# Kernel tuning notes

Measured on AMD Instinct MI355X. Metric: run time of the kernel, lower is better.

## Reference

```python
import jax, jax.numpy as jnp
import numpy as np

FEAT = 512      # feat_dim
HID = 256       # feat_dim // 2
K = 4           # DSL knn k
NCLS = 2
BUF = 8192      # rehearsal buffer size
B_BAGS = 8
N_INST = 16384


def _lin_init(k, i, o):
    return jax.random.normal(k, (i, o), jnp.float32) / np.sqrt(i)


def setup_inputs() -> dict:
    key = jax.random.key(0)
    ks = jax.random.split(key, 16)
    p = {}
    p['x'] = jax.random.normal(ks[0], (B_BAGS, N_INST, FEAT), jnp.float32)
    p['rehearsal'] = jax.random.uniform(ks[1], (BUF, FEAT), jnp.float32)
    # attention MIL pooling MLP
    p['aW1'] = _lin_init(ks[2], FEAT, FEAT); p['ab1'] = jnp.zeros((FEAT,), jnp.float32)
    p['aW2'] = _lin_init(ks[3], FEAT, 1);    p['ab2'] = jnp.zeros((1,), jnp.float32)
    # bag classifier
    p['cW'] = _lin_init(ks[4], FEAT, NCLS);  p['cb'] = jnp.zeros((NCLS,), jnp.float32)
    # DSL fc
    p['dW1'] = _lin_init(ks[5], FEAT, HID);  p['db1'] = jnp.zeros((HID,), jnp.float32)
    p['dW2'] = _lin_init(ks[6], HID, FEAT);  p['db2'] = jnp.zeros((FEAT,), jnp.float32)
    # GCN: hgc1 / hgc2 (HypergraphConv, heads=1, use_attention)
    p['g1W'] = _lin_init(ks[7], FEAT, FEAT)
    p['g1att'] = jax.random.normal(ks[8], (2 * FEAT,), jnp.float32) * 0.05
    p['g1b'] = jnp.zeros((FEAT,), jnp.float32)
    p['n1w'] = jnp.ones((FEAT,), jnp.float32); p['n1b'] = jnp.zeros((FEAT,), jnp.float32); p['n1s'] = jnp.ones((FEAT,), jnp.float32)
    p['f1W'] = _lin_init(ks[9], FEAT, HID);  p['f1b'] = jnp.zeros((HID,), jnp.float32)
    p['g2W'] = _lin_init(ks[10], FEAT, FEAT)
    p['g2att'] = jax.random.normal(ks[11], (2 * FEAT,), jnp.float32) * 0.05
    p['g2b'] = jnp.zeros((FEAT,), jnp.float32)
    p['n2w'] = jnp.ones((FEAT,), jnp.float32); p['n2b'] = jnp.zeros((FEAT,), jnp.float32); p['n2s'] = jnp.ones((FEAT,), jnp.float32)
    p['f2W'] = _lin_init(ks[12], FEAT, HID); p['f2b'] = jnp.zeros((HID,), jnp.float32)
    p['clW'] = _lin_init(ks[13], HID, NCLS); p['clb'] = jnp.zeros((NCLS,), jnp.float32)
    return p


def _hconv(x, eattr, src, edst, W, att, bias, n):
    """PyG HypergraphConv, heads=1, use_attention=True, concat, dropout=0.
    src = hyperedge_index[0] (node ids), edst = hyperedge_index[1] (hyperedge ids)."""
    xs = x @ W            # [n, F] node features after lin
    ea = eattr @ W        # [n, F] hyperedge attrs after lin
    F = xs.shape[1]
    alpha = xs[src] @ att[:F] + ea[edst] @ att[F:]        # [E]
    alpha = jax.nn.leaky_relu(alpha, 0.2)
    # softmax grouped by node index (hyperedge_index[0])
    m = jax.ops.segment_max(alpha, src, num_segments=n)
    e = jnp.exp(alpha - m[src])
    s = jax.ops.segment_sum(e, src, num_segments=n)
    alpha = e / s[src]
    ones = jnp.ones_like(alpha)
    deg = jax.ops.segment_sum(ones, src, num_segments=n)   # node degree D
    Dinv = jnp.where(deg > 0, 1.0 / deg, 0.0)
    esz = jax.ops.segment_sum(ones, edst, num_segments=n)  # hyperedge size B
    Binv = jnp.where(esz > 0, 1.0 / esz, 0.0)
    # node -> hyperedge, then hyperedge -> node
    out_e = jax.ops.segment_sum((Binv[edst] * alpha)[:, None] * xs[src], edst, num_segments=n)
    out_n = jax.ops.segment_sum((Dinv[src] * alpha)[:, None] * out_e[edst], src, num_segments=n)
    return out_n + bias


def _gnorm(x, w, b, s, eps=1e-5):
    # PyG GraphNorm, single graph
    mu = jnp.mean(x, axis=0)
    o = x - mu * s
    var = jnp.mean(o * o, axis=0)
    return w * o / jnp.sqrt(var + eps) + b


def reference(x, rehearsal, aW1, ab1, aW2, ab2, cW, cb, dW1, db1, dW2, db2,
              g1W, g1att, g1b, n1w, n1b, n1s, f1W, f1b,
              g2W, g2att, g2b, n2w, n2b, n2s, f2W, f2b, clW, clb):
    B = x.shape[0]
    # attention MIL pooling
    h = jax.nn.relu(x @ aW1 + ab1)                 # [B, N, F]
    scores = (h @ aW2 + ab2)[..., 0]               # [B, N]
    A = jax.nn.softmax(scores, axis=-1)
    M = jnp.einsum('bn,bnd->bd', A, x)             # [B, F]
    logits_mlp = M @ cW + cb
    # concat with rehearsal buffer -> graph nodes
    xc = jnp.concatenate([M, rehearsal], axis=0)   # [B+BUF, F]
    # DSL fc
    xg = jax.nn.leaky_relu(xc @ dW1 + db1, 0.01)
    xg = jax.nn.leaky_relu(xg @ dW2 + db2, 0.01)
    n = xg.shape[0]
    # cosine KNN (includes self, as torch_cluster.knn(x, x))
    xn = xg / (jnp.linalg.norm(xg, axis=1, keepdims=True) + 1e-12)
    sim = xn @ xn.T                                 # [n, n]
    _, nbr = jax.lax.top_k(sim, K)                  # [n, K]
    src = nbr.reshape(-1)                           # neighbor node ids
    edst = jnp.repeat(jnp.arange(n), K)             # hyperedge ids (query nodes)
    # scatter_mean of neighbor features per hyperedge (each has exactly K members)
    eattr = jnp.mean(xg[nbr], axis=1)               # [n, F]
    # GCN with hypergraph convs
    x1 = _hconv(xg, eattr, src, edst, g1W, g1att, g1b, n)
    x1 = jax.nn.leaky_relu(_gnorm(x1, n1w, n1b, n1s), 0.01)
    out = jax.nn.leaky_relu(x1 @ f1W + f1b, 0.01)
    x2 = _hconv(x1, eattr, src, edst, g2W, g2att, g2b, n)
    x2 = jax.nn.leaky_relu(_gnorm(x2, n2w, n2b, n2s), 0.01)
    out = out + jax.nn.leaky_relu(x2 @ f2W + f2b, 0.01)
    logits = out @ clW + clb
    logits_graph = logits[:B]
    return logits_mlp, logits_graph
```

## Files before the change

kernel.cpp:

```cpp
#include <hip/hip_runtime.h>
#include <math.h>
#include <limits.h>

#define FDIM 512
#define HIDN 256
#define NBAGS 8
#define NINST 16384
#define NNODE 8200
#define NEDGE 32800
#define BFSPLIT 8
#define MCHUNK 128

typedef __attribute__((ext_vector_type(8))) short short8v;
typedef __attribute__((ext_vector_type(4))) float f32x4v;

__device__ __forceinline__ float lrelu(float v, float s){ return v >= 0.f ? v : v*s; }

__device__ __forceinline__ void ins4(float v, int id, float* tv, int* ti){
    if ((v > tv[3]) || (v == tv[3] && id < ti[3])){
        tv[3]=v; ti[3]=id;
#pragma unroll
        for (int q=3;q>0;--q){
            bool sw = (tv[q] > tv[q-1]) || (tv[q]==tv[q-1] && ti[q]<ti[q-1]);
            if (sw){ float f=tv[q]; tv[q]=tv[q-1]; tv[q-1]=f; int d=ti[q]; ti[q]=ti[q-1]; ti[q-1]=d; }
        }
    }
}

__device__ __forceinline__ void ins8(float v, int id, float* tv, int* ti){
    if ((v > tv[7]) || (v == tv[7] && id < ti[7])){
        tv[7]=v; ti[7]=id;
#pragma unroll
        for (int q=7;q>0;--q){
            bool sw = (tv[q] > tv[q-1]) || (tv[q]==tv[q-1] && ti[q]<ti[q-1]);
            if (sw){ float f=tv[q]; tv[q]=tv[q-1]; tv[q-1]=f; int d=ti[q]; ti[q]=ti[q-1]; ti[q-1]=d; }
        }
    }
}

__device__ __forceinline__ unsigned short f2bf(float f){
    unsigned u = __float_as_uint(f);
    unsigned r = u + 0x7FFFu + ((u >> 16) & 1u);
    return (unsigned short)(r >> 16);
}
__device__ __forceinline__ float bf2f(unsigned short h){
    return __uint_as_float((unsigned)h << 16);
}

__global__ void k_wsplit(const float* __restrict__ W,
        unsigned short* __restrict__ WThi, unsigned short* __restrict__ WTlo){
    int i = blockIdx.x*256 + threadIdx.x;
    int k = i >> 9, n = i & 511;
    float w = W[i];
    unsigned short hi = f2bf(w);
    unsigned short lo = f2bf(w - bf2f(hi));
    WThi[(size_t)n*512 + k] = hi;
    WTlo[(size_t)n*512 + k] = lo;
}

__global__ __launch_bounds__(256) void k_scores(const float* __restrict__ X,
        const unsigned short* __restrict__ WThi, const unsigned short* __restrict__ WTlo,
        const float* __restrict__ b1, const float* __restrict__ v2,
        float* __restrict__ scoresP)
{
    __shared__ unsigned short Ahi[128][40];
    __shared__ unsigned short Alo[128][40];
    __shared__ unsigned short Bhi[128][40];
    __shared__ unsigned short Blo[128][40];
    int t = threadIdx.x;
    int wv = t >> 6, lane = t & 63;
    int lcol = lane & 15, lk = lane >> 4;
    size_t mb = (size_t)blockIdx.y * 128;
    int nb = blockIdx.x * 128;

    f32x4v acc[2][8];
#pragma unroll
    for (int rf=0;rf<2;rf++)
#pragma unroll
        for (int cf=0;cf<8;cf++) acc[rf][cf] = (f32x4v){0.f,0.f,0.f,0.f};

    for (int kc = 0; kc < 512; kc += 32){
        __syncthreads();
#pragma unroll
        for (int q=0;q<4;q++){
            int idx = q*256 + t;
            int seg = idx & 7, row = idx >> 3;
            float4 v = *(const float4*)(X + (mb+row)*512 + kc + seg*4);
            ushort4 h, l;
            h.x=f2bf(v.x); h.y=f2bf(v.y); h.z=f2bf(v.z); h.w=f2bf(v.w);
            l.x=f2bf(v.x-bf2f(h.x)); l.y=f2bf(v.y-bf2f(h.y));
            l.z=f2bf(v.z-bf2f(h.z)); l.w=f2bf(v.w-bf2f(h.w));
            *(ushort4*)&Ahi[row][seg*4] = h;
            *(ushort4*)&Alo[row][seg*4] = l;
        }
#pragma unroll
        for (int q=0;q<2;q++){
            int idx = q*256 + t;
            int col = idx >> 2, part = idx & 3;
            *(short8v*)&Bhi[col][part*8] =
                *(const short8v*)(WThi + (size_t)(nb+col)*512 + kc + part*8);
            *(short8v*)&Blo[col][part*8] =
                *(const short8v*)(WTlo + (size_t)(nb+col)*512 + kc + part*8);
        }
        __syncthreads();
        int r0 = wv*32;
        short8v ah0 = *(const short8v*)&Ahi[r0      + lcol][lk*8];
        short8v al0 = *(const short8v*)&Alo[r0      + lcol][lk*8];
        short8v ah1 = *(const short8v*)&Ahi[r0 + 16 + lcol][lk*8];
        short8v al1 = *(const short8v*)&Alo[r0 + 16 + lcol][lk*8];
#pragma unroll
        for (int cf=0; cf<8; cf++){
            short8v bh = *(const short8v*)&Bhi[cf*16 + lcol][lk*8];
            short8v bl = *(const short8v*)&Blo[cf*16 + lcol][lk*8];
            acc[0][cf] = __builtin_amdgcn_mfma_f32_16x16x32_bf16(ah0, bh, acc[0][cf], 0,0,0);
            acc[0][cf] = __builtin_amdgcn_mfma_f32_16x16x32_bf16(ah0, bl, acc[0][cf], 0,0,0);
            acc[0][cf] = __builtin_amdgcn_mfma_f32_16x16x32_bf16(al0, bh, acc[0][cf], 0,0,0);
            acc[1][cf] = __builtin_amdgcn_mfma_f32_16x16x32_bf16(ah1, bh, acc[1][cf], 0,0,0);
            acc[1][cf] = __builtin_amdgcn_mfma_f32_16x16x32_bf16(ah1, bl, acc[1][cf], 0,0,0);
            acc[1][cf] = __builtin_amdgcn_mfma_f32_16x16x32_bf16(al1, bh, acc[1][cf], 0,0,0);
        }
    }
    float rowsum[2][4];
#pragma unroll
    for (int rf=0;rf<2;rf++)
#pragma unroll
        for (int r=0;r<4;r++) rowsum[rf][r]=0.f;
#pragma unroll
    for (int rf=0; rf<2; rf++)
#pragma unroll
        for (int cf=0; cf<8; cf++){
            int gc = nb + cf*16 + lcol;
            float bb = b1[gc], vv = v2[gc];
#pragma unroll
            for (int r=0;r<4;r++){
                float h = acc[rf][cf][r] + bb;
                h = h > 0.f ? h : 0.f;
                rowsum[rf][r] = fmaf(h, vv, rowsum[rf][r]);
            }
        }
#pragma unroll
    for (int mask=1; mask<16; mask<<=1)
#pragma unroll
        for (int rf=0;rf<2;rf++)
#pragma unroll
            for (int r=0;r<4;r++)
                rowsum[rf][r] += __shfl_xor(rowsum[rf][r], mask);
    if (lcol == 0){
#pragma unroll
        for (int rf=0;rf<2;rf++)
#pragma unroll
            for (int r=0;r<4;r++){
                size_t grow = mb + wv*32 + rf*16 + lk*4 + r;
                scoresP[(size_t)blockIdx.x*(NBAGS*NINST) + grow] = rowsum[rf][r];
            }
    }
}

__global__ void k_scred(const float* __restrict__ sp, float* __restrict__ s){
    int r = blockIdx.x*256+threadIdx.x;
    if (r < NBAGS*NINST)
        s[r] = sp[r] + sp[NBAGS*NINST + r] + sp[2*NBAGS*NINST + r] + sp[3*NBAGS*NINST + r];
}

__global__ __launch_bounds__(256) void k_softmax(float* __restrict__ s0){
    int b = blockIdx.x; float* s = s0 + (size_t)b*NINST;
    __shared__ float red[256];
    int t = threadIdx.x;
    float m = -INFINITY;
    for (int i=t;i<NINST;i+=256) m = fmaxf(m, s[i]);
    red[t]=m; __syncthreads();
    for (int st=128; st>0; st>>=1){ if(t<st) red[t]=fmaxf(red[t],red[t+st]); __syncthreads(); }
    m = red[0]; __syncthreads();
    float sum=0.f;
    for (int i=t;i<NINST;i+=256) sum += __expf(s[i]-m);
    red[t]=sum; __syncthreads();
    for (int st=128; st>0; st>>=1){ if(t<st) red[t]+=red[t+st]; __syncthreads(); }
    float inv = 1.f/red[0];
    for (int i=t;i<NINST;i+=256) s[i] = __expf(s[i]-m)*inv;
}

__global__ __launch_bounds__(256) void k_M(const float* __restrict__ x,
        const float* __restrict__ A, float* __restrict__ MP){
    int b = blockIdx.y; int chunk = blockIdx.x;
    int n0 = chunk*(NINST/MCHUNK);
    __shared__ float As[NINST/MCHUNK];
    int t=threadIdx.x;
    if (t < NINST/MCHUNK) As[t] = A[(size_t)b*NINST+n0+t];
    __syncthreads();
    float a0=0.f, a1=0.f;
    const float* xb = x + ((size_t)b*NINST + n0)*FDIM;
    for (int n=0;n<NINST/MCHUNK;n++){
        float w = As[n];
        a0 = fmaf(w, xb[(size_t)n*FDIM + t],       a0);
        a1 = fmaf(w, xb[(size_t)n*FDIM + t + 256], a1);
    }
    MP[((size_t)chunk*NBAGS + b)*FDIM + t]       = a0;
    MP[((size_t)chunk*NBAGS + b)*FDIM + t + 256] = a1;
}

__global__ void k_Mred(const float* __restrict__ mp, float* __restrict__ M_){
    int b = blockIdx.x; int d = threadIdx.x;
    float s=0.f;
    for (int c=0;c<MCHUNK;c++) s += mp[((size_t)c*NBAGS+b)*FDIM + d];
    M_[b*FDIM+d]=s;
}

__global__ void k_logits_mlp(const float* __restrict__ M_, const float* __restrict__ cW,
        const float* __restrict__ cb, float* __restrict__ outp){
    int t = threadIdx.x;
    if (t < 16){
        int r=t>>1, c=t&1;
        float s=cb[c];
        for (int k=0;k<FDIM;k++) s = fmaf(M_[r*FDIM+k], cW[k*2+c], s);
        outp[r*2+c] = s;
    }
}

__global__ void k_xc(const float* __restrict__ M_, const float* __restrict__ reh, float* __restrict__ xc){
    size_t i = (size_t)blockIdx.x*256 + threadIdx.x;
    if (i >= (size_t)NNODE*FDIM) return;
    xc[i] = (i < (size_t)NBAGS*FDIM) ? M_[i] : reh[i - (size_t)NBAGS*FDIM];
}

__global__ __launch_bounds__(256) void k_gemm(const float* __restrict__ X,
        const float* __restrict__ W, const float* __restrict__ bias,
        float* __restrict__ C, unsigned short* __restrict__ Cbf,
        int M, int N, int K, float slope)
{
    __shared__ float As[32][68];
    __shared__ float Ws[32][128];
    int t = threadIdx.x; int tx = t & 15, ty = t >> 4;
    int mb = blockIdx.y * 64, nb = blockIdx.x * 128;
    float acc[4][8];
#pragma unroll
    for (int i=0;i<4;i++)
#pragma unroll
        for (int j=0;j<8;j++) acc[i][j]=0.f;

    int kq=(t&7)*4, m0=t>>3;
    int n4=(t&31)*4, k0=t>>5;
    for (int kc=0;kc<K;kc+=32){
#pragma unroll
        for (int mm=0;mm<2;mm++){
            int m = m0 + mm*32;
            int gr = mb + m; if (gr >= M) gr = M-1;
            float4 v = *(const float4*)(X + (size_t)gr*K + kc + kq);
            As[kq+0][m]=v.x; As[kq+1][m]=v.y; As[kq+2][m]=v.z; As[kq+3][m]=v.w;
        }
#pragma unroll
        for (int kk=0;kk<4;kk++){
            float4 v = *(const float4*)(W + (size_t)(kc+k0+kk*8)*N + nb + n4);
            *(float4*)&Ws[k0+kk*8][n4] = v;
        }
        __syncthreads();
#pragma unroll 4
        for (int k=0;k<32;k++){
            float4 a = *(const float4*)&As[k][ty*4];
            float4 b0 = *(const float4*)&Ws[k][tx*4];
            float4 b1 = *(const float4*)&Ws[k][64+tx*4];
            float av[4]={a.x,a.y,a.z,a.w};
            float bv[8]={b0.x,b0.y,b0.z,b0.w,b1.x,b1.y,b1.z,b1.w};
#pragma unroll
            for (int i=0;i<4;i++)
#pragma unroll
                for (int j=0;j<8;j++)
                    acc[i][j] = fmaf(av[i], bv[j], acc[i][j]);
        }
        __syncthreads();
    }
#pragma unroll
    for (int i=0;i<4;i++){
        int gr = mb + ty*4 + i;
        if (gr >= M) continue;
        float o[8];
#pragma unroll
        for (int j=0;j<8;j++){
            int gc = (j<4) ? (nb + tx*4 + j) : (nb + 64 + tx*4 + (j-4));
            float v = acc[i][j] + (bias ? bias[gc] : 0.f);
            o[j] = lrelu(v, slope);
        }
        float4 o0 = make_float4(o[0],o[1],o[2],o[3]);
        float4 o1 = make_float4(o[4],o[5],o[6],o[7]);
        *(float4*)(C + (size_t)gr*N + nb + tx*4)      = o0;
        *(float4*)(C + (size_t)gr*N + nb + 64 + tx*4) = o1;
        if (Cbf){
            ushort4 h0, h1;
            h0.x=f2bf(o[0]); h0.y=f2bf(o[1]); h0.z=f2bf(o[2]); h0.w=f2bf(o[3]);
            h1.x=f2bf(o[4]); h1.y=f2bf(o[5]); h1.z=f2bf(o[6]); h1.w=f2bf(o[7]);
            *(ushort4*)(Cbf + (size_t)gr*N + nb + tx*4)      = h0;
            *(ushort4*)(Cbf + (size_t)gr*N + nb + 64 + tx*4) = h1;
        }
    }
}

__global__ void k_rowdot(const float* __restrict__ X, const float* __restrict__ v,
        float* __restrict__ out, int K, int mode){
    int r = blockIdx.x; int t = threadIdx.x;
    const float* xr = X + (size_t)r*K;
    float s = 0.f;
    if (mode==1){ for (int k=t;k<K;k+=64){ float x_=xr[k]; s=fmaf(x_,x_,s);} }
    else        { for (int k=t;k<K;k+=64) s=fmaf(xr[k],v[k],s); }
    for (int off=32;off;off>>=1) s += __shfl_down(s, off);
    if (t==0) out[r] = (mode==1)? 1.f/(sqrtf(s)+1e-12f) : s;
}

__global__ void k_watt(const float* __restrict__ W, const float* __restrict__ att2, float* __restrict__ w2){
    int k = blockIdx.x; int t=threadIdx.x;
    float s=0.f;
    for (int j=t;j<FDIM;j+=64) s=fmaf(W[(size_t)k*FDIM+j], att2[j], s);
    for (int off=32;off;off>>=1) s += __shfl_down(s, off);
    if (t==0) w2[k]=s;
}

__global__ __launch_bounds__(256) void k_simbf(const unsigned short* __restrict__ xgh,
        const float* __restrict__ rn, float* __restrict__ candV, int* __restrict__ candI)
{
    __shared__ unsigned short Bs[16][520];
    int t = threadIdx.x;
    int wv = t >> 6, lane = t & 63;
    int lcol = lane & 15, lk = lane >> 4;
    int split = blockIdx.x;
    int r0 = blockIdx.y * 64 + wv * 16;

    short8v aF[16];
    {
        int arow = r0 + lcol; if (arow >= NNODE) arow = NNODE - 1;
        const unsigned short* ap = xgh + (size_t)arow * FDIM + lk * 8;
#pragma unroll
        for (int s = 0; s < 16; s++)
            aF[s] = *(const short8v*)(ap + s * 32);
    }

    int c0 = split * 1025;
    int cend = c0 + 1025;

    float tv[4][4]; int ti[4][4];
#pragma unroll
    for (int i=0;i<4;i++)
#pragma unroll
        for (int q=0;q<4;q++){ tv[i][q]=-INFINITY; ti[i][q]=INT_MAX; }

    int rho = t >> 4, seg = t & 15;

    for (int cc = c0; cc < cend; cc += 16){
        __syncthreads();
        {
            int gc = cc + rho; if (gc >= cend) gc = cend - 1;
            const unsigned short* bp = xgh + (size_t)gc * FDIM;
#pragma unroll
            for (int p = 0; p < 4; p++)
                *(short8v*)&Bs[rho][seg*8 + p*128] = *(const short8v*)(bp + seg*8 + p*128);
        }
        __syncthreads();

        f32x4v acc = {0.f, 0.f, 0.f, 0.f};
#pragma unroll
        for (int s = 0; s < 16; s++){
            short8v bF = *(const short8v*)&Bs[lcol][lk*8 + s*32];
            acc = __builtin_amdgcn_mfma_f32_16x16x32_bf16(aF[s], bF, acc, 0, 0, 0);
        }
        int gcol = cc + lcol;
        bool valid = gcol < cend;
        float rnc = valid ? rn[gcol] : 0.f;
#pragma unroll
        for (int i = 0; i < 4; i++){
            float v = valid ? acc[i] * rnc : -INFINITY;
            ins4(v, gcol, tv[i], ti[i]);
        }
    }

    float mv[4][8]; int mi[4][8];
#pragma unroll
    for (int i=0;i<4;i++){
#pragma unroll
        for (int q=0;q<4;q++){ mv[i][q]=tv[i][q]; mi[i][q]=ti[i][q]; }
#pragma unroll
        for (int q=4;q<8;q++){ mv[i][q]=-INFINITY; mi[i][q]=INT_MAX; }
    }
#pragma unroll
    for (int mask=1; mask<16; mask<<=1){
        float ov[4][8]; int oi[4][8];
#pragma unroll
        for (int i=0;i<4;i++)
#pragma unroll
            for (int q=0;q<8;q++){
                ov[i][q] = __shfl_xor(mv[i][q], mask);
                oi[i][q] = __shfl_xor(mi[i][q], mask);
            }
#pragma unroll
        for (int i=0;i<4;i++)
#pragma unroll
            for (int q=0;q<8;q++)
                ins8(ov[i][q], oi[i][q], mv[i], mi[i]);
    }
    if (lcol == 0){
#pragma unroll
        for (int i=0;i<4;i++){
            int grow = r0 + lk*4 + i;
            if (grow < NNODE){
#pragma unroll
                for (int q=0;q<8;q++){
                    candV[((size_t)grow*BFSPLIT + split)*8 + q] = mv[i][q];
                    candI[((size_t)grow*BFSPLIT + split)*8 + q] = mi[i][q];
                }
            }
        }
    }
}

__global__ __launch_bounds__(256) void k_rescore(const float* __restrict__ xg,
        const float* __restrict__ rn, const float* __restrict__ candV,
        const int* __restrict__ candI, int* __restrict__ nbr)
{
    __shared__ float Xr[4][512];
    __shared__ float Cs[256][17];
    __shared__ int   CrowS[256];
    int t = threadIdx.x;
    int wv = t >> 6, lane = t & 63;
    int r0 = blockIdx.x * 4;
    int r  = r0 + wv;
    int cid = candI[(size_t)r*64 + lane];
    float pv = candV[(size_t)r*64 + lane];
    bool ok = (pv != -INFINITY) && (cid >= 0) && (cid < NNODE);
    int crow = ok ? cid : 0;
    CrowS[t] = crow;
    {
        int rr = t >> 6; int c = t & 63;
        const float* xp = xg + (size_t)(r0+rr)*FDIM;
        *(float4*)&Xr[rr][c*4]       = *(const float4*)(xp + c*4);
        *(float4*)&Xr[rr][256 + c*4] = *(const float4*)(xp + 256 + c*4);
    }
    float dot = 0.f;
    for (int kc = 0; kc < 512; kc += 16){
        __syncthreads();
#pragma unroll
        for (int p = 0; p < 4; p++){
            int slot = p*64 + (t >> 2);
            int f = t & 3;
            float4 v = *(const float4*)(xg + (size_t)CrowS[slot]*FDIM + kc + f*4);
            float* dst = &Cs[slot][f*4];
            dst[0]=v.x; dst[1]=v.y; dst[2]=v.z; dst[3]=v.w;
        }
        __syncthreads();
#pragma unroll
        for (int k2 = 0; k2 < 16; k2++)
            dot = fmaf(Xr[wv][kc + k2], Cs[t][k2], dot);
    }
    float v = ok ? (dot * rn[r]) * rn[crow] : -INFINITY;
    int id = ok ? cid : INT_MAX;
    float tvv[4]={-INFINITY,-INFINITY,-INFINITY,-INFINITY};
    int tii[4]={INT_MAX,INT_MAX,INT_MAX,INT_MAX};
    ins4(v, id, tvv, tii);
#pragma unroll
    for (int mask=1; mask<64; mask<<=1){
        float ov[4]; int oi[4];
#pragma unroll
        for (int s=0;s<4;s++){ ov[s]=__shfl_xor(tvv[s],mask); oi[s]=__shfl_xor(tii[s],mask); }
#pragma unroll
        for (int s=0;s<4;s++) ins4(ov[s], oi[s], tvv, tii);
    }
    if (lane == 0){
#pragma unroll
        for (int s=0;s<4;s++) nbr[r*4+s] = tii[s];
    }
}

__global__ void k_eattr(const float* __restrict__ xg, const int* __restrict__ nbr, float* __restrict__ ea){
    int j = blockIdx.x; int t = threadIdx.x;
    int n0=nbr[j*4], n1=nbr[j*4+1], n2=nbr[j*4+2], n3=nbr[j*4+3];
    for (int d=t; d<FDIM; d+=256){
        float s = xg[(size_t)n0*FDIM+d]+xg[(size_t)n1*FDIM+d]+xg[(size_t)n2*FDIM+d]+xg[(size_t)n3*FDIM+d];
        ea[(size_t)j*FDIM+d] = 0.25f*s;
    }
}

__global__ void k_count(const int* __restrict__ nbr, int* __restrict__ counts){
    int e = blockIdx.x*256+threadIdx.x; if(e<NEDGE) atomicAdd(&counts[nbr[e]],1);
}

__global__ void k_scan(const int* __restrict__ counts, int* __restrict__ csrOff){
    __shared__ int part[257];
    int t=threadIdx.x;
    int start = t*33; int s=0;
    for (int i=0;i<33;i++){ int idx=start+i; if(idx<NNODE) s += counts[idx]; }
    part[t+1]=s; if(t==0) part[0]=0;
    __syncthreads();
    if (t==0){ for (int i=1;i<=256;i++) part[i]+=part[i-1]; }
    __syncthreads();
    int run = part[t];
    for (int i=0;i<33;i++){ int idx=start+i; if(idx<NNODE){ csrOff[idx]=run; run+=counts[idx]; } }
    if (t==255) csrOff[NNODE]=run;
}

__global__ void k_fill(const int* __restrict__ nbr, const int* __restrict__ csrOff,
        int* __restrict__ fillPos, int* __restrict__ csrE){
    int e = blockIdx.x*256+threadIdx.x; if(e>=NEDGE) return;
    int i = nbr[e];
    int p = atomicAdd(&fillPos[i],1);
    csrE[csrOff[i]+p] = e;
}

__global__ void k_alpha(const int* __restrict__ nbr, const float* __restrict__ ps,
        const float* __restrict__ pe, float* __restrict__ alphan){
    int e = blockIdx.x*256+threadIdx.x; if(e>=NEDGE) return;
    float a = ps[nbr[e]] + pe[e>>2];
    alphan[e] = a>=0.f? a : 0.2f*a;
}

__global__ void k_esm(const int* __restrict__ csrOff, const int* __restrict__ csrE,
        float* __restrict__ alphan){
    int i = blockIdx.x*256+threadIdx.x; if(i>=NNODE) return;
    int s0=csrOff[i], s1=csrOff[i+1];
    if (s1==s0) return;
    float m=-INFINITY;
    for (int s=s0;s<s1;s++) m = fmaxf(m, alphan[csrE[s]]);
    float Z=0.f;
    for (int s=s0;s<s1;s++) Z += __expf(alphan[csrE[s]]-m);
    float inv = 1.f/Z;
    for (int s=s0;s<s1;s++){ int e=csrE[s]; alphan[e] = __expf(alphan[e]-m)*inv; }
}

__global__ void k_oute(const float* __restrict__ xs, const float* __restrict__ alphan,
        const int* __restrict__ nbr, float* __restrict__ out_e){
    int j = blockIdx.x; int t=threadIdx.x;
    __shared__ float a[4]; __shared__ int sidx[4];
    if (t<4){ a[t]=alphan[j*4+t]; sidx[t]=nbr[j*4+t]; }
    __syncthreads();
    for (int d=t; d<FDIM; d+=256){
        float v = a[0]*xs[(size_t)sidx[0]*FDIM+d] + a[1]*xs[(size_t)sidx[1]*FDIM+d]
                + a[2]*xs[(size_t)sidx[2]*FDIM+d] + a[3]*xs[(size_t)sidx[3]*FDIM+d];
        out_e[(size_t)j*FDIM+d] = 0.25f*v;
    }
}

__global__ void k_outn(const float* __restrict__ out_e, const float* __restrict__ alphan,
        const int* __restrict__ csrOff, const int* __restrict__ csrE,
        const float* __restrict__ bias, float* __restrict__ out_n){
    int i = blockIdx.x; int t=threadIdx.x;
    int s0=csrOff[i], s1=csrOff[i+1];
    float Dinv = (s1>s0)? 1.f/(float)(s1-s0) : 0.f;
    for (int d=t; d<FDIM; d+=256){
        float accv=0.f;
        for (int s=s0;s<s1;s++){
            int e=csrE[s];
            accv = fmaf(alphan[e], out_e[(size_t)(e>>2)*FDIM+d], accv);
        }
        out_n[(size_t)i*FDIM+d] = bias[d] + Dinv*accv;
    }
}

__global__ void k_colstat1(const float* __restrict__ Xn, float* __restrict__ p1, float* __restrict__ p2){
    int b = blockIdx.x; int t=threadIdx.x;
    float s0=0,q0=0,s1=0,q1=0;
    for (int r=b; r<NNODE; r+=64){
        float v0 = Xn[(size_t)r*FDIM + t];
        float v1 = Xn[(size_t)r*FDIM + t + 256];
        s0+=v0; q0=fmaf(v0,v0,q0); s1+=v1; q1=fmaf(v1,v1,q1);
    }
    p1[b*FDIM+t]=s0; p1[b*FDIM+t+256]=s1;
    p2[b*FDIM+t]=q0; p2[b*FDIM+t+256]=q1;
}

__global__ void k_colstat2(const float* __restrict__ p1, const float* __restrict__ p2,
        const float* __restrict__ w, const float* __restrict__ sc,
        float* __restrict__ mu, float* __restrict__ g){
    int d = threadIdx.x + blockIdx.x*256; if(d>=FDIM) return;
    float s=0,q=0;
    for (int bb=0;bb<64;bb++){ s+=p1[bb*FDIM+d]; q+=p2[bb*FDIM+d]; }
    float m = s/(float)NNODE;
    float ms = m*sc[d];
    float var = q/(float)NNODE - 2.f*ms*m + ms*ms;
    mu[d]=m;
    g[d] = w[d]*rsqrtf(var+1e-5f);
}

__global__ void k_gnapply(const float* __restrict__ Xin, const float* __restrict__ mu,
        const float* __restrict__ g, const float* __restrict__ sc,
        const float* __restrict__ bb, float* __restrict__ Xout){
    size_t i = (size_t)blockIdx.x*256+threadIdx.x;
    if (i >= (size_t)NNODE*FDIM) return;
    int d = (int)(i & 511);
    float o = Xin[i] - mu[d]*sc[d];
    Xout[i] = lrelu(g[d]*o + bb[d], 0.01f);
}

__global__ void k_final(const float* __restrict__ x1, const float* __restrict__ x2,
        const float* __restrict__ f1W, const float* __restrict__ f1b,
        const float* __restrict__ f2W, const float* __restrict__ f2b,
        const float* __restrict__ clW, const float* __restrict__ clb,
        float* __restrict__ outp){
    int r = blockIdx.x;
    int h = threadIdx.x;
    __shared__ float o8[HIDN];
    float s1=f1b[h], s2=f2b[h];
    for (int k=0;k<FDIM;k++){
        s1 = fmaf(x1[(size_t)r*FDIM+k], f1W[(size_t)k*HIDN+h], s1);
        s2 = fmaf(x2[(size_t)r*FDIM+k], f2W[(size_t)k*HIDN+h], s2);
    }
    o8[h] = lrelu(s1,0.01f)+lrelu(s2,0.01f);
    __syncthreads();
    if (h < 2){
        float s = clb[h];
        for (int k=0;k<HIDN;k++) s = fmaf(o8[k], clW[k*2+h], s);
        outp[16 + r*2 + h] = s;
    }
}

extern "C" void kernel_launch(void* const* d_in, const int* in_sizes, int n_in,
                              void* d_out, int out_size, void* d_ws, size_t ws_size,
                              hipStream_t stream) {
    (void)in_sizes; (void)n_in; (void)out_size; (void)ws_size;
    const float* x    = (const float*)d_in[0];
    const float* reh  = (const float*)d_in[1];
    const float* aW1  = (const float*)d_in[2];
    const float* ab1  = (const float*)d_in[3];
    const float* aW2  = (const float*)d_in[4];
    const float* cW   = (const float*)d_in[6];
    const float* cb   = (const float*)d_in[7];
    const float* dW1  = (const float*)d_in[8];
    const float* db1  = (const float*)d_in[9];
    const float* dW2  = (const float*)d_in[10];
    const float* db2  = (const float*)d_in[11];
    const float* g1W  = (const float*)d_in[12];
    const float* g1att= (const float*)d_in[13];
    const float* g1b  = (const float*)d_in[14];
    const float* n1w  = (const float*)d_in[15];
    const float* n1b  = (const float*)d_in[16];
    const float* n1s  = (const float*)d_in[17];
    const float* f1W  = (const float*)d_in[18];
    const float* f1b  = (const float*)d_in[19];
    const float* g2W  = (const float*)d_in[20];
    const float* g2att= (const float*)d_in[21];
    const float* g2b  = (const float*)d_in[22];
    const float* n2w  = (const float*)d_in[23];
    const float* n2b  = (const float*)d_in[24];
    const float* n2s  = (const float*)d_in[25];
    const float* f2W  = (const float*)d_in[26];
    const float* f2b  = (const float*)d_in[27];
    const float* clW  = (const float*)d_in[28];
    const float* clb  = (const float*)d_in[29];
    float* out = (float*)d_out;
    char* ws = (char*)d_ws;

    float* scores = (float*)(ws + 0);
    float* Mbuf   = (float*)(ws + 524288);
    float* xc     = (float*)(ws + 540672);
    float* xg1    = (float*)(ws + 17334272);
    float* xg     = (float*)(ws + 25731072);
    float* rn     = (float*)(ws + 42524672);
    int*   nbrp   = (int*)  (ws + 44656896);
    float* eattr  = (float*)(ws + 44788224);
    int*   counts = (int*)  (ws + 61581824);
    int*   csrOff = (int*)  (ws + 61614848);
    int*   fillPos= (int*)  (ws + 61647872);
    int*   csrE   = (int*)  (ws + 61680896);
    float* w2     = (float*)(ws + 61812096);
    float* ps     = (float*)(ws + 61814144);
    float* pe     = (float*)(ws + 61847040);
    float* alphan = (float*)(ws + 61880064);
    float* out_e  = (float*)(ws + 62011264);
    float* out_n  = (float*)(ws + 78804864);
    float* part1  = (float*)(ws + 95598464);
    float* part2  = (float*)(ws + 95729536);
    float* mu     = (float*)(ws + 95860608);
    float* gsc    = (float*)(ws + 95862656);
    float* x1buf  = (float*)(ws + 95864704);
    float* scoresP= (float*)(ws + 112658304);
    float* xs     = xc;
    float* x2buf  = xg;
    float* MP     = scoresP;
    unsigned short* WThi = (unsigned short*)eattr;
    unsigned short* WTlo = (unsigned short*)((char*)eattr + 524288);
    unsigned short* xgh = (unsigned short*)out_e;
    int*   candI  = (int*)((char*)out_e + 8396800);
    float* candV  = out_n;

    hipMemsetAsync(counts, 0, NNODE*sizeof(int), stream);
    hipMemsetAsync(fillPos, 0, NNODE*sizeof(int), stream);

    k_wsplit<<<1024,256,0,stream>>>(aW1, WThi, WTlo);
    k_scores<<<dim3(4,1024),256,0,stream>>>(x, WThi, WTlo, ab1, aW2, scoresP);
    k_scred<<<512,256,0,stream>>>(scoresP, scores);
    k_softmax<<<NBAGS,256,0,stream>>>(scores);
    k_M<<<dim3(MCHUNK,NBAGS),256,0,stream>>>(x, scores, MP);
    k_Mred<<<NBAGS,512,0,stream>>>(MP, Mbuf);
    k_logits_mlp<<<1,64,0,stream>>>(Mbuf, cW, cb, out);

    k_xc<<<(NNODE*FDIM+255)/256,256,0,stream>>>(Mbuf, reh, xc);
    k_gemm<<<dim3(2,(NNODE+63)/64),256,0,stream>>>(xc, dW1, db1, xg1, nullptr, NNODE, HIDN, FDIM, 0.01f);
    k_gemm<<<dim3(4,(NNODE+63)/64),256,0,stream>>>(xg1, dW2, db2, xg, xgh, NNODE, FDIM, HIDN, 0.01f);

    k_rowdot<<<NNODE,64,0,stream>>>(xg, nullptr, rn, FDIM, 1);
    k_simbf<<<dim3(BFSPLIT,(NNODE+63)/64),256,0,stream>>>(xgh, rn, candV, candI);
    k_rescore<<<NNODE/4,256,0,stream>>>(xg, rn, candV, candI, nbrp);
    k_eattr<<<NNODE,256,0,stream>>>(xg, nbrp, eattr);
    k_count<<<(NEDGE+255)/256,256,0,stream>>>(nbrp, counts);
    k_scan<<<1,256,0,stream>>>(counts, csrOff);
    k_fill<<<(NEDGE+255)/256,256,0,stream>>>(nbrp, csrOff, fillPos, csrE);

    for (int layer=0; layer<2; ++layer){
        const float* Xin  = layer==0 ? xg   : x1buf;
        const float* W    = layer==0 ? g1W  : g2W;
        const float* att  = layer==0 ? g1att: g2att;
        const float* gb   = layer==0 ? g1b  : g2b;
        const float* nw   = layer==0 ? n1w  : n2w;
        const float* nb_  = layer==0 ? n1b  : n2b;
        const float* ns   = layer==0 ? n1s  : n2s;
        float* Xout       = layer==0 ? x1buf: x2buf;

        k_gemm<<<dim3(4,(NNODE+63)/64),256,0,stream>>>(Xin, W, nullptr, xs, nullptr, NNODE, FDIM, FDIM, 1.0f);
        k_watt<<<FDIM,64,0,stream>>>(W, att+FDIM, w2);
        k_rowdot<<<NNODE,64,0,stream>>>(xs, att, ps, FDIM, 0);
        k_rowdot<<<NNODE,64,0,stream>>>(eattr, w2, pe, FDIM, 0);
        k_alpha<<<(NEDGE+255)/256,256,0,stream>>>(nbrp, ps, pe, alphan);
        k_esm<<<(NNODE+255)/256,256,0,stream>>>(csrOff, csrE, alphan);
        k_oute<<<NNODE,256,0,stream>>>(xs, alphan, nbrp, out_e);
        k_outn<<<NNODE,256,0,stream>>>(out_e, alphan, csrOff, csrE, gb, out_n);
        k_colstat1<<<64,256,0,stream>>>(out_n, part1, part2);
        k_colstat2<<<2,256,0,stream>>>(part1, part2, nw, ns, mu, gsc);
        k_gnapply<<<(NNODE*FDIM+255)/256,256,0,stream>>>(out_n, mu, gsc, ns, nb_, Xout);
    }

    k_final<<<NBAGS,HIDN,0,stream>>>(x1buf, x2buf, f1W, f1b, f2W, f2b, clW, clb, out);
}
```

Baseline: 1.687 ms.

## Use split-bf16 MFMA GEMM for hconv and widen KNN split parallelism

Adds a k_gemm3 kernel that computes the hypergraph-conv X@W products with three bf16 MFMA passes (hi*hi, hi*lo, lo*hi) on pre-split weights, replacing the previous fp32 GEMM. The brute-force similarity kernel now uses 16 column splits instead of 8 and two independent accumulators to shorten the MFMA dependency chain. Because this doubles the candidate count, rescoring runs in two halves and a merge kernel combines the partial top-4 lists. The split-bf16 GEMM gives slightly different rounding from fp32, and the extra launches and weight-split passes add some overhead.

```diff
diff --git a/kernel.cpp b/kernel.cpp
--- a/kernel.cpp
+++ b/kernel.cpp
@@ -8,7 +8,8 @@
 #define NINST 16384
 #define NNODE 8200
 #define NEDGE 32800
-#define BFSPLIT 8
+#define BFSPLIT 16
+#define SPLITW 513
 #define MCHUNK 128
 
 typedef __attribute__((ext_vector_type(8))) short short8v;
@@ -154,6 +155,86 @@
                 scoresP[(size_t)blockIdx.x*(NBAGS*NINST) + grow] = rowsum[rf][r];
             }
     }
+}
+
+__global__ __launch_bounds__(256) void k_gemm3(const float* __restrict__ X,
+        const unsigned short* __restrict__ WThi, const unsigned short* __restrict__ WTlo,
+        const float* __restrict__ bias, float* __restrict__ C,
+        int M, int N, int K, float slope)
+{
+    __shared__ unsigned short Ahi[128][40];
+    __shared__ unsigned short Alo[128][40];
+    __shared__ unsigned short Bhi[128][40];
+    __shared__ unsigned short Blo[128][40];
+    int t = threadIdx.x;
+    int wv = t >> 6, lane = t & 63;
+    int lcol = lane & 15, lk = lane >> 4;
+    int mb = blockIdx.y * 128;
+    int nb = blockIdx.x * 128;
+
+    f32x4v acc[2][8];
+#pragma unroll
+    for (int rf=0;rf<2;rf++)
+#pragma unroll
+        for (int cf=0;cf<8;cf++) acc[rf][cf] = (f32x4v){0.f,0.f,0.f,0.f};
+
+    for (int kc = 0; kc < K; kc += 32){
+        __syncthreads();
+#pragma unroll
+        for (int q=0;q<4;q++){
+            int idx = q*256 + t;
+            int seg = idx & 7, row = idx >> 3;
+            int gr = mb + row; if (gr >= M) gr = M-1;
+            float4 v = *(const float4*)(X + (size_t)gr*K + kc + seg*4);
+            ushort4 h, l;
+            h.x=f2bf(v.x); h.y=f2bf(v.y); h.z=f2bf(v.z); h.w=f2bf(v.w);
+            l.x=f2bf(v.x-bf2f(h.x)); l.y=f2bf(v.y-bf2f(h.y));
+            l.z=f2bf(v.z-bf2f(h.z)); l.w=f2bf(v.w-bf2f(h.w));
+            *(ushort4*)&Ahi[row][seg*4] = h;
+            *(ushort4*)&Alo[row][seg*4] = l;
+        }
+#pragma unroll
+        for (int q=0;q<2;q++){
+            int idx = q*256 + t;
+            int col = idx >> 2, part = idx & 3;
+            *(short8v*)&Bhi[col][part*8] =
+                *(const short8v*)(WThi + (size_t)(nb+col)*K + kc + part*8);
+            *(short8v*)&Blo[col][part*8] =
+                *(const short8v*)(WTlo + (size_t)(nb+col)*K + kc + part*8);
+        }
+        __syncthreads();
+        int r0 = wv*32;
+        short8v ah0 = *(const short8v*)&Ahi[r0      + lcol][lk*8];
+        short8v al0 = *(const short8v*)&Alo[r0      + lcol][lk*8];
+        short8v ah1 = *(const short8v*)&Ahi[r0 + 16 + lcol][lk*8];
+        short8v al1 = *(const short8v*)&Alo[r0 + 16 + lcol][lk*8];
+#pragma unroll
+        for (int cf=0; cf<8; cf++){
+            short8v bh = *(const short8v*)&Bhi[cf*16 + lcol][lk*8];
+            short8v bl = *(const short8v*)&Blo[cf*16 + lcol][lk*8];
+            acc[0][cf] = __builtin_amdgcn_mfma_f32_16x16x32_bf16(ah0, bh, acc[0][cf], 0,0,0);
+            acc[0][cf] = __builtin_amdgcn_mfma_f32_16x16x32_bf16(ah0, bl, acc[0][cf], 0,0,0);
+            acc[0][cf] = __builtin_amdgcn_mfma_f32_16x16x32_bf16(al0, bh, acc[0][cf], 0,0,0);
+            acc[1][cf] = __builtin_amdgcn_mfma_f32_16x16x32_bf16(ah1, bh, acc[1][cf], 0,0,0);
+            acc[1][cf] = __builtin_amdgcn_mfma_f32_16x16x32_bf16(ah1, bl, acc[1][cf], 0,0,0);
+            acc[1][cf] = __builtin_amdgcn_mfma_f32_16x16x32_bf16(al1, bh, acc[1][cf], 0,0,0);
+        }
+    }
+#pragma unroll
+    for (int rf=0; rf<2; rf++)
+#pragma unroll
+        for (int cf=0; cf<8; cf++){
+            int gc = nb + cf*16 + lcol;
+            float bb = bias ? bias[gc] : 0.f;
+#pragma unroll
+            for (int r=0;r<4;r++){
+                int grow = mb + wv*32 + rf*16 + lk*4 + r;
+                if (grow < M){
+                    float v = acc[rf][cf][r] + bb;
+                    C[(size_t)grow*N + gc] = lrelu(v, slope);
+                }
+            }
+        }
 }
 
 __global__ void k_scred(const float* __restrict__ sp, float* __restrict__ s){
@@ -331,8 +412,8 @@
             aF[s] = *(const short8v*)(ap + s * 32);
     }
 
-    int c0 = split * 1025;
-    int cend = c0 + 1025;
+    int c0 = split * SPLITW;
+    int cend = c0 + SPLITW; if (cend > NNODE) cend = NNODE;
 
     float tv[4][4]; int ti[4][4];
 #pragma unroll
@@ -353,18 +434,21 @@
         }
         __syncthreads();
 
-        f32x4v acc = {0.f, 0.f, 0.f, 0.f};
-#pragma unroll
-        for (int s = 0; s < 16; s++){
-            short8v bF = *(const short8v*)&Bs[lcol][lk*8 + s*32];
-            acc = __builtin_amdgcn_mfma_f32_16x16x32_bf16(aF[s], bF, acc, 0, 0, 0);
+        f32x4v acc0 = {0.f,0.f,0.f,0.f};
+        f32x4v acc1 = {0.f,0.f,0.f,0.f};
+#pragma unroll
+        for (int s = 0; s < 8; s++){
+            short8v b0 = *(const short8v*)&Bs[lcol][lk*8 + s*32];
+            short8v b1 = *(const short8v*)&Bs[lcol][lk*8 + (s+8)*32];
+            acc0 = __builtin_amdgcn_mfma_f32_16x16x32_bf16(aF[s],   b0, acc0, 0, 0, 0);
+            acc1 = __builtin_amdgcn_mfma_f32_16x16x32_bf16(aF[s+8], b1, acc1, 0, 0, 0);
         }
         int gcol = cc + lcol;
         bool valid = gcol < cend;
         float rnc = valid ? rn[gcol] : 0.f;
 #pragma unroll
         for (int i = 0; i < 4; i++){
-            float v = valid ? acc[i] * rnc : -INFINITY;
+            float v = valid ? (acc0[i] + acc1[i]) * rnc : -INFINITY;
             ins4(v, gcol, tv[i], ti[i]);
         }
     }
@@ -410,7 +494,8 @@
 
 __global__ __launch_bounds__(256) void k_rescore(const float* __restrict__ xg,
         const float* __restrict__ rn, const float* __restrict__ candV,
-        const int* __restrict__ candI, int* __restrict__ nbr)
+        const int* __restrict__ candI, int half,
+        float* __restrict__ htV, int* __restrict__ htI)
 {
     __shared__ float Xr[4][512];
     __shared__ float Cs[256][17];
@@ -419,8 +504,8 @@
     int wv = t >> 6, lane = t & 63;
     int r0 = blockIdx.x * 4;
     int r  = r0 + wv;
-    int cid = candI[(size_t)r*64 + lane];
-    float pv = candV[(size_t)r*64 + lane];
+    int cid = candI[(size_t)r*128 + half*64 + lane];
+    float pv = candV[(size_t)r*128 + half*64 + lane];
     bool ok = (pv != -INFINITY) && (cid >= 0) && (cid < NNODE);
     int crow = ok ? cid : 0;
     CrowS[t] = crow;
@@ -461,8 +546,19 @@
     }
     if (lane == 0){
 #pragma unroll
-        for (int s=0;s<4;s++) nbr[r*4+s] = tii[s];
-    }
+        for (int s=0;s<4;s++){ htV[r*8 + half*4 + s] = tvv[s]; htI[r*8 + half*4 + s] = tii[s]; }
+    }
+}
+
+__global__ void k_hmerge(const float* __restrict__ htV, const int* __restrict__ htI,
+        int* __restrict__ nbr){
+    int r = blockIdx.x*256+threadIdx.x; if (r>=NNODE) return;
+    float tv[4]={-INFINITY,-INFINITY,-INFINITY,-INFINITY};
+    int ti[4]={INT_MAX,INT_MAX,INT_MAX,INT_MAX};
+#pragma unroll
+    for (int q=0;q<8;q++) ins4(htV[r*8+q], htI[r*8+q], tv, ti);
+#pragma unroll
+    for (int s=0;s<4;s++) nbr[r*4+s] = ti[s];
 }
 
 __global__ void k_eattr(const float* __restrict__ xg, const int* __restrict__ nbr, float* __restrict__ ea){
@@ -669,11 +765,17 @@
     float* xs     = xc;
     float* x2buf  = xg;
     float* MP     = scoresP;
+    unsigned short* gW1hi = (unsigned short*)scoresP;
+    unsigned short* gW1lo = (unsigned short*)((char*)scoresP + 524288);
+    unsigned short* gW2hi = (unsigned short*)((char*)scoresP + 1048576);
+    unsigned short* gW2lo = (unsigned short*)((char*)scoresP + 1572864);
     unsigned short* WThi = (unsigned short*)eattr;
     unsigned short* WTlo = (unsigned short*)((char*)eattr + 524288);
     unsigned short* xgh = (unsigned short*)out_e;
-    int*   candI  = (int*)((char*)out_e + 8396800);
-    float* candV  = out_n;
+    int*   candI = (int*)((char*)out_e + 8396800);
+    int*   htI   = (int*)((char*)out_e + 12595200);
+    float* candV = out_n;
+    float* htV   = (float*)((char*)out_n + 4198400);
 
     hipMemsetAsync(counts, 0, NNODE*sizeof(int), stream);
     hipMemsetAsync(fillPos, 0, NNODE*sizeof(int), stream);
@@ -686,13 +788,18 @@
     k_Mred<<<NBAGS,512,0,stream>>>(MP, Mbuf);
     k_logits_mlp<<<1,64,0,stream>>>(Mbuf, cW, cb, out);
 
+    k_wsplit<<<1024,256,0,stream>>>(g1W, gW1hi, gW1lo);
+    k_wsplit<<<1024,256,0,stream>>>(g2W, gW2hi, gW2lo);
+
     k_xc<<<(NNODE*FDIM+255)/256,256,0,stream>>>(Mbuf, reh, xc);
     k_gemm<<<dim3(2,(NNODE+63)/64),256,0,stream>>>(xc, dW1, db1, xg1, nullptr, NNODE, HIDN, FDIM, 0.01f);
     k_gemm<<<dim3(4,(NNODE+63)/64),256,0,stream>>>(xg1, dW2, db2, xg, xgh, NNODE, FDIM, HIDN, 0.01f);
 
     k_rowdot<<<NNODE,64,0,stream>>>(xg, nullptr, rn, FDIM, 1);
     k_simbf<<<dim3(BFSPLIT,(NNODE+63)/64),256,0,stream>>>(xgh, rn, candV, candI);
-    k_rescore<<<NNODE/4,256,0,stream>>>(xg, rn, candV, candI, nbrp);
+    k_rescore<<<NNODE/4,256,0,stream>>>(xg, rn, candV, candI, 0, htV, htI);
+    k_rescore<<<NNODE/4,256,0,stream>>>(xg, rn, candV, candI, 1, htV, htI);
+    k_hmerge<<<(NNODE+255)/256,256,0,stream>>>(htV, htI, nbrp);
     k_eattr<<<NNODE,256,0,stream>>>(xg, nbrp, eattr);
     k_count<<<(NEDGE+255)/256,256,0,stream>>>(nbrp, counts);
     k_scan<<<1,256,0,stream>>>(counts, csrOff);
@@ -701,6 +808,8 @@
     for (int layer=0; layer<2; ++layer){
         const float* Xin  = layer==0 ? xg   : x1buf;
         const float* W    = layer==0 ? g1W  : g2W;
+        const unsigned short* Whi = layer==0 ? gW1hi : gW2hi;
+        const unsigned short* Wlo = layer==0 ? gW1lo : gW2lo;
         const float* att  = layer==0 ? g1att: g2att;
         const float* gb   = layer==0 ? g1b  : g2b;
         const float* nw   = layer==0 ? n1w  : n2w;
@@ -708,7 +817,7 @@
         const float* ns   = layer==0 ? n1s  : n2s;
         float* Xout       = layer==0 ? x1buf: x2buf;
 
-        k_gemm<<<dim3(4,(NNODE+63)/64),256,0,stream>>>(Xin, W, nullptr, xs, nullptr, NNODE, FDIM, FDIM, 1.0f);
+        k_gemm3<<<dim3(4,(NNODE+127)/128),256,0,stream>>>(Xin, Whi, Wlo, nullptr, xs, NNODE, FDIM, FDIM, 1.0f);
         k_watt<<<FDIM,64,0,stream>>>(W, att+FDIM, w2);
         k_rowdot<<<NNODE,64,0,stream>>>(xs, att, ps, FDIM, 0);
         k_rowdot<<<NNODE,64,0,stream>>>(eattr, w2, pe, FDIM, 0);
```

Result: no change. 1.654 ms (-1.9%).
